# Kernel tuning notes

Hardware: AMD Instinct MI355X
Metric: run time of the kernel (lower is better)

Reference implementation:

```python
import jax, jax.numpy as jnp
import numpy as np

NCLASSES = 21
CONF_THRESH = 0.5
IOU_THRESH = 0.45
TOP_K = 200
NMS_MAX_OUT = 400
NEG = jnp.float32(-1e9)  # sentinel for suppressed / below-threshold scores

B, N_BOXES = 8, 8732
LAST = NCLASSES + 4 * (NCLASSES - 1) + 1  # 102


def setup_inputs() -> dict:
    key = jax.random.key(0)
    kc, kxy, kwh, ke = jax.random.split(key, 4)
    conf = jax.random.uniform(kc, (B, N_BOXES, NCLASSES), dtype=jnp.float32)
    # plausible normalized boxes: xmin,ymin in [0,0.8], width/height in [0.01,0.2]
    xy = jax.random.uniform(kxy, (B, N_BOXES, NCLASSES - 1, 2), minval=0.0, maxval=0.8)
    wh = jax.random.uniform(kwh, (B, N_BOXES, NCLASSES - 1, 2), minval=0.01, maxval=0.2)
    boxes = jnp.concatenate([xy, xy + wh], axis=-1).reshape(B, N_BOXES, 4 * (NCLASSES - 1))
    extra = jax.random.uniform(ke, (B, N_BOXES, 1), dtype=jnp.float32)
    y_pred = jnp.concatenate([conf, boxes, extra], axis=-1)  # [B, N, 102]
    return {"y_pred": y_pred}


def _iou_one_vs_all(box, boxes):
    # box: [4] (xmin,ymin,xmax,ymax); boxes: [N,4]
    x1 = jnp.maximum(box[0], boxes[:, 0])
    y1 = jnp.maximum(box[1], boxes[:, 1])
    x2 = jnp.minimum(box[2], boxes[:, 2])
    y2 = jnp.minimum(box[3], boxes[:, 3])
    inter = jnp.maximum(x2 - x1, 0.0) * jnp.maximum(y2 - y1, 0.0)
    area_a = (box[2] - box[0]) * (box[3] - box[1])
    area_b = (boxes[:, 2] - boxes[:, 0]) * (boxes[:, 3] - boxes[:, 1])
    union = area_a + area_b - inter
    return jnp.where(union > 0.0, inter / union, 0.0)


def _nms_one_class(rows):
    # rows: [N, 7] = (class_id, conf, xmin, ymin, xmax, ymax, extra)
    n = rows.shape[0]
    scores0 = jnp.where(rows[:, 1] > CONF_THRESH, rows[:, 1], NEG)
    boxes = rows[:, 2:6]
    idx_range = jnp.arange(n)

    def step(live, _):
        best = jnp.argmax(live)
        valid = live[best] > NEG * 0.5  # any real score passed the threshold
        ious = _iou_one_vs_all(boxes[best], boxes)
        suppress = valid & ((ious > IOU_THRESH) | (idx_range == best))
        live = jnp.where(suppress, NEG, live)
        return live, (best, valid)

    _, (sel, selv) = jax.lax.scan(step, scores0, None, length=NMS_MAX_OUT)
    # gather selected rows; zero-pad invalid slots (matches tf.pad with 0)
    out = jnp.where(selv[:, None], rows[sel], 0.0)  # [NMS_MAX_OUT, 7]
    return out


def _per_image(item):
    # item: [N, 102]
    n = item.shape[0]
    conf = item[:, 1:NCLASSES]                                  # [N, C-1]
    boxes = item[:, NCLASSES:NCLASSES + 4 * (NCLASSES - 1)].reshape(n, NCLASSES - 1, 4)
    extra = item[:, -1]                                         # [N]
    class_ids = jnp.arange(1, NCLASSES, dtype=item.dtype)       # [C-1]
    rows = jnp.concatenate([
        jnp.broadcast_to(class_ids[:, None, None], (NCLASSES - 1, n, 1)),
        conf.T[:, :, None],
        jnp.transpose(boxes, (1, 0, 2)),
        jnp.broadcast_to(extra[None, :, None], (NCLASSES - 1, n, 1)),
    ], axis=-1)                                                 # [C-1, N, 7]
    per_class = jax.vmap(_nms_one_class)(rows)                  # [C-1, MAX_OUT, 7]
    filtered = per_class.reshape(-1, 7)                         # [(C-1)*MAX_OUT, 7]
    _, top_idx = jax.lax.top_k(filtered[:, 1], TOP_K)           # sorted descending
    return filtered[top_idx]                                    # [TOP_K, 7]


def reference(y_pred):
    return jax.vmap(_per_image)(y_pred)  # [B, TOP_K, 7]
```

## Files before the change

### kernel.cpp

```cpp
#include <hip/hip_runtime.h>
#include <cstdint>

#define NB 8
#define NBOX 8732
#define NCL 21
#define NCM1 20
#define LASTD 102
#define CONF_TH 0.5f
#define IOU_TH 0.45f
#define TOPK 200
#define MAXOUT 400
#define SELCAP 200
#define EMITN 256
#define NTASK (NB * NCM1)
#define THREADS 1024
#define NW 16
#define NIT 9
#define NBIN 2048
#define KPAD 8768
#define NBATCH (KPAD / 64)
#define CPAD 8736

#define MIDD ((double)IOU_TH + 0x1p-26)


struct SM {
    float4 selbox[SELCAP];
    float selA[SELCAP];
    uint64_t selkey[SELCAP];
    uint64_t keys[KPAD];
    uint64_t smask[2][64];
    unsigned long long extC[2];
    int hist[NBIN];
    int binstart[NBIN];
    int wavetot[NW];
    int Mshare, nselshare, prevNshare, doneflag;
};

__device__ __forceinline__ int iou_sup(float4 a, float aA, float4 b, float bA) {
    float x1 = fmaxf(a.x, b.x), y1 = fmaxf(a.y, b.y);
    float x2 = fminf(a.z, b.z), y2 = fminf(a.w, b.w);
    float iw = fmaxf(__fsub_rn(x2, x1), 0.0f);
    float ih = fmaxf(__fsub_rn(y2, y1), 0.0f);
    float inter = __fmul_rn(iw, ih);
    float uni = __fsub_rn(__fadd_rn(aA, bA), inter);
    return (double)inter > MIDD * (double)uni;
}

__device__ __forceinline__ float4 load_box(const float* __restrict__ img,
                                           int boxoff, uint64_t key) {
    if ((key >> 32) == 0) return make_float4(0.f, 0.f, 0.f, 0.f);
    uint32_t i = 0xFFFFFFFFu - (uint32_t)key;
    const float* bp = img + (size_t)i * LASTD + boxoff;
    return make_float4(bp[0], bp[1], bp[2], bp[3]);
}

__device__ __forceinline__ float box_area(float4 b) {
    return __fmul_rn(__fsub_rn(b.z, b.x), __fsub_rn(b.w, b.y));
}

__device__ __forceinline__ float4 shfl_box(float4 b, int c) {
    float4 r;
    r.x = __shfl(b.x, c); r.y = __shfl(b.y, c);
    r.z = __shfl(b.z, c); r.w = __shfl(b.w, c);
    return r;
}

__global__ __launch_bounds__(256) void transpose_conf(const float* __restrict__ yp,
                                                      float* __restrict__ confT,
                                                      float* __restrict__ extraT) {
    const uint32_t TOT4 = (uint32_t)NB * NBOX * LASTD / 4u;
    for (uint32_t i4 = blockIdx.x * blockDim.x + threadIdx.x; i4 < TOT4;
         i4 += gridDim.x * blockDim.x) {
        float4 v = ((const float4*)yp)[i4];
        uint32_t base = i4 * 4u;
        #pragma unroll
        for (int k = 0; k < 4; ++k) {
            uint32_t flat = base + k;
            uint32_t b = flat / (NBOX * LASTD);
            uint32_t rem = flat - b * (NBOX * LASTD);
            uint32_t row = rem / LASTD;
            uint32_t col = rem - row * LASTD;
            float f = (k == 0) ? v.x : (k == 1) ? v.y : (k == 2) ? v.z : v.w;
            if (col - 1u < (uint32_t)NCM1)
                confT[((size_t)b * NCM1 + (col - 1u)) * CPAD + row] = f;
            else if (col == LASTD - 1)
                extraT[(size_t)b * CPAD + row] = f;
        }
    }
}

__device__ void build_keys(const float* __restrict__ confsrc, int cstride,
                           SM& sm, int tid, int lane, int wav) {
    float confs[NIT];
    #pragma unroll
    for (int it = 0; it < NIT; ++it) {
        int idx = it * THREADS + tid;
        confs[it] = (idx < NBOX) ? confsrc[(size_t)idx * cstride] : 0.0f;
    }
    sm.hist[tid] = 0; sm.hist[tid + THREADS] = 0;
    __syncthreads();

    #pragma unroll
    for (int it = 0; it < NIT; ++it) {
        int idx = it * THREADS + tid;
        if (idx < NBOX && confs[it] > CONF_TH) {
            int bin = (int)((__float_as_uint(confs[it]) - 0x3F000000u) >> 12);
            atomicAdd(&sm.hist[bin], 1);
        }
    }
    __syncthreads();

    int h0 = sm.hist[2 * tid], h1 = sm.hist[2 * tid + 1];
    int x = h0 + h1;
    int s = x;
    #pragma unroll
    for (int d = 1; d <= 32; d <<= 1) {
        int y = __shfl_down(s, d);
        if (lane + d < 64) s += y;
    }
    if (lane == 0) sm.wavetot[wav] = s;
    __syncthreads();
    int cross = 0;
    #pragma unroll
    for (int w = 0; w < NW; ++w)
        if (w > wav) cross += sm.wavetot[w];
    int Safter = cross + s - x;
    sm.binstart[2 * tid + 1] = Safter;
    sm.binstart[2 * tid] = Safter + h1;
    if (tid == 0) sm.Mshare = cross + s;
    sm.hist[2 * tid] = 0; sm.hist[2 * tid + 1] = 0;
    __syncthreads();

    #pragma unroll
    for (int it = 0; it < NIT; ++it) {
        int idx = it * THREADS + tid;
        if (idx < NBOX && confs[it] > CONF_TH) {
            uint32_t bits = __float_as_uint(confs[it]);
            int bin = (int)((bits - 0x3F000000u) >> 12);
            int slot = sm.binstart[bin] + atomicAdd(&sm.hist[bin], 1);
            sm.keys[slot] = ((uint64_t)bits << 32) |
                            (uint32_t)(0xFFFFFFFFu - (uint32_t)idx);
        }
    }
    __syncthreads();
    const int M = sm.Mshare;
    for (int m = M + tid; m < KPAD; m += THREADS) sm.keys[m] = 0;
    for (int f = tid; f < NBIN; f += THREADS) {
        int s0 = sm.binstart[f], h = sm.hist[f];
        for (int i2 = 1; i2 < h; ++i2) {
            uint64_t key = sm.keys[s0 + i2];
            int j = i2 - 1;
            while (j >= 0 && sm.keys[s0 + j] < key) {
                sm.keys[s0 + j + 1] = sm.keys[s0 + j];
                --j;
            }
            sm.keys[s0 + j + 1] = key;
        }
    }
    __syncthreads();
}

__device__ int greedy_scan(const float* __restrict__ img, int boxoff, SM& sm,
                           int tid, int lane, int wav) {
    uint64_t keyC = sm.keys[lane];
    uint64_t keyN = sm.keys[64 + lane];
    float4 boxC = load_box(img, boxoff, keyC);
    float4 boxN = load_box(img, boxoff, keyN);
    float aC = box_area(boxC), aN = box_area(boxN);
    #pragma unroll
    for (int tt = 0; tt < 4; ++tt) {
        int c = wav + tt * NW;
        float4 cb = shfl_box(boxC, c);
        float ca = __shfl(aC, c);
        uint64_t row = 0;
        if (ca > 0.0f)
            row = __ballot(lane < c && iou_sup(cb, ca, boxC, aC));
        if (lane == 0) sm.smask[0][c] = row;
    }
    if (tid == 0) { sm.extC[0] = 0ull; sm.extC[1] = 0ull; }
    __syncthreads();

    int nsel = 0, prevN = 0;
    bool done = false;
    for (int i = 0; i < NBATCH && !done; ++i) {
        const int p = i & 1;
        const bool vC = (keyC >> 32) != 0;
        {
            int sup = 0;
            for (int j = prevN + wav; j < nsel; j += NW)
                sup |= iou_sup(boxC, aC, sm.selbox[j], sm.selA[j]);
            unsigned long long bal = __ballot(vC && sup);
            if (lane == 0 && bal) atomicOr(&sm.extC[p], bal);
        }
        int f0 = (i + 2) * 64;
        uint64_t key2 = (f0 < KPAD) ? sm.keys[f0 + lane] : 0;
        float4 box2 = load_box(img, boxoff, key2);
        float a2 = box_area(box2);
        __syncthreads();
        const int nselPre = nsel;
        if (wav == 0) {
            unsigned long long V = __ballot(vC);
            unsigned long long E = sm.extC[p];
            if (lane == 0) sm.extC[p] = 0ull;
            uint64_t smc = sm.smask[p][lane];
            uint64_t alive = ~(E | ~V);
            uint64_t accm = 0;
            int cnt = nsel;
            while (alive && cnt < SELCAP) {
                int t = __ffsll((unsigned long long)alive) - 1;
                uint64_t bit = 1ull << t;
                accm |= bit;
                cnt++;
                unsigned long long kill = __ballot((smc >> t) & 1ull);
                alive &= ~(kill | bit);
            }
            if ((accm >> lane) & 1ull) {
                int pos = nsel + __popcll(accm & ((1ull << lane) - 1ull));
                sm.selbox[pos] = boxC;
                sm.selA[pos] = aC;
                sm.selkey[pos] = keyC;
            }
            if (lane == 0) {
                sm.nselshare = cnt;
                sm.prevNshare = nsel;
                sm.doneflag = (cnt >= SELCAP) || (V != ~0ull);
            }
        } else {
            float4 cb[5];
            float ca[5];
            unsigned amask = 0;
            #pragma unroll
            for (int k = 0; k < 5; ++k) {
                int c = (wav - 1) + k * (NW - 1);
                float4 t4 = make_float4(0.f, 0.f, 0.f, 0.f);
                float tA = 0.0f;
                if (c < 64) {
                    t4 = shfl_box(boxN, c);
                    tA = __shfl(aN, c);
                }
                cb[k] = t4; ca[k] = tA;
                if (c < 64 && tA > 0.0f) amask |= 1u << k;
            }
            unsigned long long sb = 0;
            for (int j0 = 0; j0 < nselPre && amask; j0 += 64) {
                int j = j0 + lane;
                bool jv = j < nselPre;
                float4 sbx = sm.selbox[jv ? j : 0];
                float sA = sm.selA[jv ? j : 0];
                #pragma unroll
                for (int k = 0; k < 5; ++k) {
                    if (!((amask >> k) & 1u)) continue;
                    int hit = jv && iou_sup(cb[k], ca[k], sbx, sA);
                    if (__ballot(hit)) {
                        amask &= ~(1u << k);
                        sb |= 1ull << ((wav - 1) + k * (NW - 1));
                    }
                }
            }
            #pragma unroll
            for (int k = 0; k < 5; ++k) {
                if (!((amask >> k) & 1u)) continue;
                int c = (wav - 1) + k * (NW - 1);
                uint64_t row = __ballot(lane < c && iou_sup(cb[k], ca[k], boxN, aN));
                if (lane == 0) sm.smask[p ^ 1][c] = row;
            }
            if (lane == 0 && sb) atomicOr(&sm.extC[p ^ 1], sb);
        }
        __syncthreads();
        nsel = sm.nselshare;
        prevN = sm.prevNshare;
        done = sm.doneflag != 0;
        keyC = keyN; boxC = boxN; aC = aN;
        keyN = key2; boxN = box2; aN = a2;
    }
    return nsel;
}

__device__ void emit_rows(const float* __restrict__ extrasrc, int estride,
                          int cm1, SM& sm, int nsel, float* __restrict__ rows,
                          int task, int tid) {
    float* out0 = rows + (size_t)task * MAXOUT * 7;
    for (int r = tid; r < EMITN; r += THREADS) {
        float* o = out0 + (size_t)r * 7;
        if (r < nsel) {
            uint64_t key = sm.selkey[r];
            uint32_t i = 0xFFFFFFFFu - (uint32_t)key;
            float4 bx = sm.selbox[r];
            o[0] = (float)(cm1 + 1);
            o[1] = __uint_as_float((uint32_t)(key >> 32));
            o[2] = bx.x;
            o[3] = bx.y;
            o[4] = bx.z;
            o[5] = bx.w;
            o[6] = extrasrc[(size_t)i * estride];
        } else {
            #pragma unroll
            for (int q = 0; q < 7; ++q) o[q] = 0.0f;
        }
    }
}

__global__ __launch_bounds__(THREADS) void nms_fast(const float* __restrict__ yp,
                                                    const float* __restrict__ confT,
                                                    const float* __restrict__ extraT,
                                                    float* __restrict__ rows) {
    __shared__ SM sm;
    const int task = blockIdx.x;
    const int b = task / NCM1;
    const int cm1 = task % NCM1;
    const int tid = threadIdx.x;
    const float* img = yp + (size_t)b * NBOX * LASTD;
    build_keys(confT + (size_t)task * CPAD, 1, sm, tid, tid & 63, tid >> 6);
    int nsel = greedy_scan(img, NCL + 4 * cm1, sm, tid, tid & 63, tid >> 6);
    emit_rows(extraT + (size_t)b * CPAD, 1, cm1, sm, nsel, rows, task, tid);
}

__global__ __launch_bounds__(THREADS) void nms_mono(const float* __restrict__ yp,
                                                    float* __restrict__ rows) {
    __shared__ SM sm;
    const int task = blockIdx.x;
    const int b = task / NCM1;
    const int cm1 = task % NCM1;
    const int tid = threadIdx.x;
    const float* img = yp + (size_t)b * NBOX * LASTD;
    build_keys(img + 1 + cm1, LASTD, sm, tid, tid & 63, tid >> 6);
    int nsel = greedy_scan(img, NCL + 4 * cm1, sm, tid, tid & 63, tid >> 6);
    emit_rows(img + (LASTD - 1), LASTD, cm1, sm, nsel, rows, task, tid);
}

__global__ __launch_bounds__(THREADS) void topk_per_image(const float* __restrict__ rows,
                                                          float* __restrict__ out) {
    __shared__ uint64_t K[8192];
    const int b = blockIdx.x;
    const int tid = threadIdx.x;
    const float* rb = rows + (size_t)b * (NCM1 * MAXOUT) * 7;

    for (int xx = tid; xx < 8192; xx += THREADS) {
        int list = xx >> 8, r = xx & 255;
        uint64_t k = 0;
        if (list < NCM1) {
            int flat = list * MAXOUT + r;
            float conf = rb[(size_t)flat * 7 + 1];
            k = ((uint64_t)__float_as_uint(conf) << 32) |
                (uint32_t)(0xFFFFFFFFu - (uint32_t)flat);
        }
        K[xx] = k;
    }
    __syncthreads();

    for (int round = 0; round < 5; ++round) {
        int npairs = 16 >> round;
        int sep = 256 << round;
        for (int w = tid; w < npairs * 256; w += THREADS) {
            int p = w >> 8, t = w & 255;
            int A = p * 2 * sep;
            uint64_t a = K[A + t];
            uint64_t c = K[A + sep + 255 - t];
            K[A + t] = a > c ? a : c;
        }
        __syncthreads();
        for (int j = 128; j >= 1; j >>= 1) {
            for (int w = tid; w < npairs * 128; w += THREADS) {
                int p = w >> 7, q = w & 127;
                int t = ((q & ~(j - 1)) << 1) | (q & (j - 1));
                int A = p * 2 * sep;
                uint64_t x0 = K[A + t];
                uint64_t x1 = K[A + t + j];
                if (x0 < x1) { K[A + t] = x1; K[A + t + j] = x0; }
            }
            __syncthreads();
        }
    }

    if (tid < TOPK) {
        uint64_t key = K[tid];
        uint32_t flat = 0xFFFFFFFFu - (uint32_t)key;
        const float* src = rb + (size_t)flat * 7;
        float* o = out + ((size_t)b * TOPK + tid) * 7;
        #pragma unroll
        for (int q = 0; q < 7; ++q) o[q] = src[q];
    }
}

extern "C" void kernel_launch(void* const* d_in, const int* in_sizes, int n_in,
                              void* d_out, int out_size, void* d_ws, size_t ws_size,
                              hipStream_t stream) {
    const float* yp = (const float*)d_in[0];
    float* rows = (float*)d_ws;
    const size_t rowsB = (size_t)NTASK * MAXOUT * 7 * sizeof(float);
    float* confT = (float*)((char*)d_ws + rowsB);
    const size_t confB = (size_t)NTASK * CPAD * sizeof(float);
    float* extraT = (float*)((char*)confT + confB);
    const size_t extraB = (size_t)NB * CPAD * sizeof(float);
    const size_t need = rowsB + confB + extraB;
    float* out = (float*)d_out;

    if (ws_size >= need) {
        hipLaunchKernelGGL(transpose_conf, dim3(2048), dim3(256), 0, stream,
                           yp, confT, extraT);
        hipLaunchKernelGGL(nms_fast, dim3(NTASK), dim3(THREADS), 0, stream,
                           yp, confT, extraT, rows);
    } else {
        hipLaunchKernelGGL(nms_mono, dim3(NTASK), dim3(THREADS), 0, stream,
                           yp, rows);
    }
    hipLaunchKernelGGL(topk_per_image, dim3(NB), dim3(THREADS), 0, stream,
                       rows, out);
}
```

Baseline: 65.22 us.

## Add truncated top-1024 NMS fast path with fallback; shuffle-based bitonic tail in topk

The NMS kernel first builds a sorted key list holding only the top ~1024 candidates by score bin, then runs the greedy scan over that short list. It falls back to the full build and scan when the truncated list cannot be shown to yield the same result (fewer than SELCAP selections while candidates were dropped). This avoids sorting and scanning all above-threshold boxes in the common case. Separately, the topk bitonic merge replaces the last six shared-memory stages with in-register wavefront xor shuffles, cutting barriers and LDS traffic. The risk is redoing the whole build and scan when the fallback triggers, plus added template code.

Result: faster. 59.34 us (-9.0%).

```diff
diff --git a/kernel.cpp b/kernel.cpp
--- a/kernel.cpp
+++ b/kernel.cpp
@@ -19,6 +19,9 @@
 #define NBIN 2048
 #define KPAD 8768
 #define NBATCH (KPAD / 64)
+#define NTR 1024
+#define KPAD_TR (NTR + 64)
+#define NBATCH_TR (KPAD_TR / 64)
 #define CPAD 8736
 
 #define MIDD ((double)IOU_TH + 0x1p-26)
@@ -34,7 +37,7 @@
     int hist[NBIN];
     int binstart[NBIN];
     int wavetot[NW];
-    int Mshare, nselshare, prevNshare, doneflag;
+    int Mshare, MtrShare, nselshare, prevNshare, doneflag;
 };
 
 __device__ __forceinline__ int iou_sup(float4 a, float aA, float4 b, float bA) {
@@ -64,6 +67,10 @@
     r.x = __shfl(b.x, c); r.y = __shfl(b.y, c);
     r.z = __shfl(b.z, c); r.w = __shfl(b.w, c);
     return r;
+}
+
+__device__ __forceinline__ uint64_t shfl_xor_u64(uint64_t v, int m) {
+    return (uint64_t)__shfl_xor((unsigned long long)v, m, 64);
 }
 
 __global__ __launch_bounds__(256) void transpose_conf(const float* __restrict__ yp,
@@ -90,8 +97,11 @@
     }
 }
 
-__device__ void build_keys(const float* __restrict__ confsrc, int cstride,
-                           SM& sm, int tid, int lane, int wav) {
+template <bool TRM>
+__device__ void build_keys_impl(const float* __restrict__ confsrc, int cstride,
+                                SM& sm, int tid, int lane, int wav,
+                                int& M, int& Mtr) {
+    constexpr int PADT = TRM ? KPAD_TR : KPAD;
     float confs[NIT];
     #pragma unroll
     for (int it = 0; it < NIT; ++it) {
@@ -99,6 +109,7 @@
         confs[it] = (idx < NBOX) ? confsrc[(size_t)idx * cstride] : 0.0f;
     }
     sm.hist[tid] = 0; sm.hist[tid + THREADS] = 0;
+    if (tid == 0) sm.MtrShare = 0;
     __syncthreads();
 
     #pragma unroll
@@ -129,8 +140,17 @@
     sm.binstart[2 * tid + 1] = Safter;
     sm.binstart[2 * tid] = Safter + h1;
     if (tid == 0) sm.Mshare = cross + s;
+    if (TRM) {
+        int cand = 0;
+        if (Safter < NTR && h1 > 0) cand = Safter + h1;
+        int bs0 = Safter + h1;
+        if (bs0 < NTR && h0 > 0) { int c2 = bs0 + h0; cand = cand > c2 ? cand : c2; }
+        if (cand > 0) atomicMax(&sm.MtrShare, cand);
+    }
     sm.hist[2 * tid] = 0; sm.hist[2 * tid + 1] = 0;
     __syncthreads();
+    M = sm.Mshare;
+    Mtr = TRM ? sm.MtrShare : M;
 
     #pragma unroll
     for (int it = 0; it < NIT; ++it) {
@@ -138,16 +158,20 @@
         if (idx < NBOX && confs[it] > CONF_TH) {
             uint32_t bits = __float_as_uint(confs[it]);
             int bin = (int)((bits - 0x3F000000u) >> 12);
-            int slot = sm.binstart[bin] + atomicAdd(&sm.hist[bin], 1);
-            sm.keys[slot] = ((uint64_t)bits << 32) |
-                            (uint32_t)(0xFFFFFFFFu - (uint32_t)idx);
-        }
-    }
-    __syncthreads();
-    const int M = sm.Mshare;
-    for (int m = M + tid; m < KPAD; m += THREADS) sm.keys[m] = 0;
+            if (!TRM || sm.binstart[bin] < NTR) {
+                int slot = sm.binstart[bin] + atomicAdd(&sm.hist[bin], 1);
+                if (!TRM || slot < PADT)
+                    sm.keys[slot] = ((uint64_t)bits << 32) |
+                                    (uint32_t)(0xFFFFFFFFu - (uint32_t)idx);
+            }
+        }
+    }
+    __syncthreads();
+    int Mp = Mtr < PADT ? Mtr : PADT;
+    for (int m = Mp + tid; m < PADT; m += THREADS) sm.keys[m] = 0;
     for (int f = tid; f < NBIN; f += THREADS) {
         int s0 = sm.binstart[f], h = sm.hist[f];
+        if (TRM && (s0 >= NTR || s0 + h > PADT)) continue;
         for (int i2 = 1; i2 < h; ++i2) {
             uint64_t key = sm.keys[s0 + i2];
             int j = i2 - 1;
@@ -161,6 +185,7 @@
     __syncthreads();
 }
 
+template <int KPADT, int NBATCHT>
 __device__ int greedy_scan(const float* __restrict__ img, int boxoff, SM& sm,
                            int tid, int lane, int wav) {
     uint64_t keyC = sm.keys[lane];
@@ -183,7 +208,7 @@
 
     int nsel = 0, prevN = 0;
     bool done = false;
-    for (int i = 0; i < NBATCH && !done; ++i) {
+    for (int i = 0; i < NBATCHT && !done; ++i) {
         const int p = i & 1;
         const bool vC = (keyC >> 32) != 0;
         {
@@ -194,7 +219,7 @@
             if (lane == 0 && bal) atomicOr(&sm.extC[p], bal);
         }
         int f0 = (i + 2) * 64;
-        uint64_t key2 = (f0 < KPAD) ? sm.keys[f0 + lane] : 0;
+        uint64_t key2 = (f0 < KPADT) ? sm.keys[f0 + lane] : 0;
         float4 box2 = load_box(img, boxoff, key2);
         float a2 = box_area(box2);
         __syncthreads();
@@ -310,9 +335,23 @@
     const int b = task / NCM1;
     const int cm1 = task % NCM1;
     const int tid = threadIdx.x;
+    const int lane = tid & 63;
+    const int wav = tid >> 6;
     const float* img = yp + (size_t)b * NBOX * LASTD;
-    build_keys(confT + (size_t)task * CPAD, 1, sm, tid, tid & 63, tid >> 6);
-    int nsel = greedy_scan(img, NCL + 4 * cm1, sm, tid, tid & 63, tid >> 6);
+    const float* conf = confT + (size_t)task * CPAD;
+    const int boxoff = NCL + 4 * cm1;
+
+    int M, Mtr;
+    build_keys_impl<true>(conf, 1, sm, tid, lane, wav, M, Mtr);
+    int nsel = -1;
+    if (Mtr <= KPAD_TR) {
+        nsel = greedy_scan<KPAD_TR, NBATCH_TR>(img, boxoff, sm, tid, lane, wav);
+        if (nsel < SELCAP && Mtr < M) nsel = -1;
+    }
+    if (nsel < 0) {
+        build_keys_impl<false>(conf, 1, sm, tid, lane, wav, M, Mtr);
+        nsel = greedy_scan<KPAD, NBATCH>(img, boxoff, sm, tid, lane, wav);
+    }
     emit_rows(extraT + (size_t)b * CPAD, 1, cm1, sm, nsel, rows, task, tid);
 }
 
@@ -324,8 +363,11 @@
     const int cm1 = task % NCM1;
     const int tid = threadIdx.x;
     const float* img = yp + (size_t)b * NBOX * LASTD;
-    build_keys(img + 1 + cm1, LASTD, sm, tid, tid & 63, tid >> 6);
-    int nsel = greedy_scan(img, NCL + 4 * cm1, sm, tid, tid & 63, tid >> 6);
+    int M, Mtr;
+    build_keys_impl<false>(img + 1 + cm1, LASTD, sm, tid, tid & 63, tid >> 6,
+                           M, Mtr);
+    int nsel = greedy_scan<KPAD, NBATCH>(img, NCL + 4 * cm1, sm, tid,
+                                         tid & 63, tid >> 6);
     emit_rows(img + (LASTD - 1), LASTD, cm1, sm, nsel, rows, task, tid);
 }
 
@@ -360,7 +402,7 @@
             K[A + t] = a > c ? a : c;
         }
         __syncthreads();
-        for (int j = 128; j >= 1; j >>= 1) {
+        for (int j = 128; j >= 64; j >>= 1) {
             for (int w = tid; w < npairs * 128; w += THREADS) {
                 int p = w >> 7, q = w & 127;
                 int t = ((q & ~(j - 1)) << 1) | (q & (j - 1));
@@ -371,6 +413,20 @@
             }
             __syncthreads();
         }
+        for (int w = tid; w < npairs * 256; w += THREADS) {
+            int p = w >> 8, t = w & 255;
+            int xI = p * 2 * sep + t;
+            uint64_t v = K[xI];
+            #pragma unroll
+            for (int j = 32; j >= 1; j >>= 1) {
+                uint64_t pr = shfl_xor_u64(v, j);
+                uint64_t mx = v > pr ? v : pr;
+                uint64_t mn = v > pr ? pr : v;
+                v = ((t & j) == 0) ? mx : mn;
+            }
+            K[xI] = v;
+        }
+        __syncthreads();
     }
 
     if (tid < TOPK) {
```
